# Kernel optimization log

Hardware: AMD Instinct MI355X
Metric: run time of the kernel (lower is better)

The kernel has to match this reference:

```python
import jax, jax.numpy as jnp
import numpy as np
import math

N_HEAD = 16
EPS = 1e-5
GELU_C = math.sqrt(2.0 / math.pi)

def _layernorm(v, w):
    # LN with weight only (bias=None), matching the module's quirky constructor
    mu = jnp.mean(v, axis=-1, keepdims=True)
    var = jnp.mean(jnp.square(v - mu), axis=-1, keepdims=True)
    return (v - mu) * jax.lax.rsqrt(var + EPS) * w

def _new_gelu(x):
    return 0.5 * x * (1.0 + jnp.tanh(GELU_C * (x + 0.044715 * x ** 3)))

def setup_inputs() -> dict:
    key = jax.random.key(0)
    k1, k2, k3, k4 = jax.random.split(key, 4)
    B, T, C = 2, 2048, 2048
    x = jax.random.normal(k1, (B, T, C), dtype=jnp.float32)
    w_qkv = jax.random.normal(k2, (C, 3 * C), dtype=jnp.float32) * 0.02
    w1 = jax.random.normal(k3, (C, 4 * C), dtype=jnp.float32) * 0.02
    w2 = jax.random.normal(k4, (4 * C, C), dtype=jnp.float32) * 0.02
    ln_w = jnp.ones((C,), dtype=jnp.float32)
    return {"x": x, "w_qkv": w_qkv, "w1": w1, "w2": w2, "ln_w": ln_w}

def reference(x, w_qkv, w1, w2, ln_w):
    B, T, C = x.shape
    H = N_HEAD
    D = C // H
    # --- attention branch (pre-LN, shared ln weight) ---
    h = _layernorm(x, ln_w)
    qkv = h @ w_qkv  # [B,T,3C]
    q, k, v = jnp.split(qkv, 3, axis=-1)
    q = q.reshape(B, T, H, D)
    k = k.reshape(B, T, H, D)
    v = v.reshape(B, T, H, D)
    scale = 1.0 / math.sqrt(D)
    att = jnp.einsum('bthd,bshd->bhts', q, k) * scale  # [B,H,T,T]
    causal = jnp.tril(jnp.ones((T, T), dtype=bool))
    att = jnp.where(causal, att, -jnp.inf)
    att = jax.nn.softmax(att, axis=-1)
    attn_out = jnp.einsum('bhts,bshd->bthd', att, v).reshape(B, T, C)
    x = x + attn_out  # note: no output projection in this module
    # --- MLP branch (same ln weight reused) ---
    h2 = _layernorm(x, ln_w)
    mlp = _new_gelu(h2 @ w1) @ w2
    return x + mlp
```

## Files before the change

kernel.cpp:

```cpp
#include <hip/hip_runtime.h>
#include <hip/hip_bf16.h>
#include <math.h>

typedef __bf16 BF16;
typedef __attribute__((ext_vector_type(8))) __bf16 bf16x8;
typedef __attribute__((ext_vector_type(4))) float f32x4;

__device__ __forceinline__ void gld_lds16(const void* g, void* l) {
    __builtin_amdgcn_global_load_lds(
        (__attribute__((address_space(1))) void*)(const void*)g,
        (__attribute__((address_space(3))) void*)l, 16, 0, 0);
}

template <int N> __device__ __forceinline__ void vmwait() {
    if constexpr (N == 0) asm volatile("s_waitcnt vmcnt(0)" ::: "memory");
    else if constexpr (N == 2) asm volatile("s_waitcnt vmcnt(2)" ::: "memory");
    else if constexpr (N == 3) asm volatile("s_waitcnt vmcnt(3)" ::: "memory");
    else if constexpr (N == 4) asm volatile("s_waitcnt vmcnt(4)" ::: "memory");
    else if constexpr (N == 6) asm volatile("s_waitcnt vmcnt(6)" ::: "memory");
    else if constexpr (N == 8) asm volatile("s_waitcnt vmcnt(8)" ::: "memory");
}

__device__ __forceinline__ void barrier_() {
    asm volatile("" ::: "memory");
    __builtin_amdgcn_s_barrier();
    asm volatile("" ::: "memory");
}

__global__ __launch_bounds__(256) void lnorm(const float* __restrict__ x,
                                             const float* __restrict__ w,
                                             BF16* __restrict__ out) {
    const int row = blockIdx.x, tid = threadIdx.x;
    const float* xr = x + (size_t)row * 2048;
    float4 a = *(const float4*)(xr + tid * 8);
    float4 b = *(const float4*)(xr + tid * 8 + 4);
    float s1 = a.x + a.y + a.z + a.w + b.x + b.y + b.z + b.w;
    float s2 = a.x*a.x + a.y*a.y + a.z*a.z + a.w*a.w +
               b.x*b.x + b.y*b.y + b.z*b.z + b.w*b.w;
    #pragma unroll
    for (int off = 32; off; off >>= 1) {
        s1 += __shfl_xor(s1, off);
        s2 += __shfl_xor(s2, off);
    }
    __shared__ float red[8];
    const int l = tid & 63, wv = tid >> 6;
    if (l == 0) { red[wv] = s1; red[4 + wv] = s2; }
    __syncthreads();
    s1 = red[0] + red[1] + red[2] + red[3];
    s2 = red[4] + red[5] + red[6] + red[7];
    const float mean = s1 * (1.0f / 2048.0f);
    const float var  = s2 * (1.0f / 2048.0f) - mean * mean;
    const float rstd = rsqrtf(var + 1e-5f);
    float4 wa = *(const float4*)(w + tid * 8);
    float4 wb = *(const float4*)(w + tid * 8 + 4);
    bf16x8 o;
    o[0] = (BF16)((a.x - mean) * rstd * wa.x);
    o[1] = (BF16)((a.y - mean) * rstd * wa.y);
    o[2] = (BF16)((a.z - mean) * rstd * wa.z);
    o[3] = (BF16)((a.w - mean) * rstd * wa.w);
    o[4] = (BF16)((b.x - mean) * rstd * wb.x);
    o[5] = (BF16)((b.y - mean) * rstd * wb.y);
    o[6] = (BF16)((b.z - mean) * rstd * wb.z);
    o[7] = (BF16)((b.w - mean) * rstd * wb.w);
    *(bf16x8*)(out + (size_t)row * 2048 + tid * 8) = o;
}

__global__ __launch_bounds__(256) void wtrans(const float* __restrict__ W,
                                              BF16* __restrict__ Wt,
                                              int K, int N) {
    __shared__ BF16 tile[32][33];
    const int n0 = blockIdx.x * 32, k0 = blockIdx.y * 32;
    const int tx = threadIdx.x, ty = threadIdx.y;
    #pragma unroll
    for (int i = 0; i < 4; i++)
        tile[ty + 8 * i][tx] = (BF16)W[(size_t)(k0 + ty + 8 * i) * N + n0 + tx];
    __syncthreads();
    #pragma unroll
    for (int i = 0; i < 4; i++)
        Wt[(size_t)(n0 + ty + 8 * i) * K + k0 + tx] = tile[tx][ty + 8 * i];
}

__global__ __launch_bounds__(256) void vtrans(const BF16* __restrict__ qkv,
                                              BF16* __restrict__ vT) {
    __shared__ BF16 tile[32][33];
    const int t0 = blockIdx.x * 32, d0 = blockIdx.y * 32, bh = blockIdx.z;
    const int b = bh >> 4, h = bh & 15;
    const int tx = threadIdx.x, ty = threadIdx.y;
    const BF16* src = qkv + (size_t)b * 2048 * 6144 + 4096 + h * 128;
    #pragma unroll
    for (int i = 0; i < 4; i++)
        tile[ty + 8 * i][tx] = src[(size_t)(t0 + ty + 8 * i) * 6144 + d0 + tx];
    __syncthreads();
    BF16* dst = vT + (size_t)bh * 128 * 2048;
    #pragma unroll
    for (int i = 0; i < 4; i++)
        dst[(size_t)(d0 + ty + 8 * i) * 2048 + t0 + tx] = tile[tx][ty + 8 * i];
}

#define STAGE_A(SB, TS) do { \
    gld_lds16(gA + (size_t)(TS) * 32, lA + (SB) * ABUF); \
    if (LA == 2) gld_lds16(gA + (size_t)(TS) * 32 + (size_t)128 * K, \
                           lA + (SB) * ABUF + 4096); \
} while (0)

#define STAGE_B(SB, TS) do { \
    gld_lds16(gB + (size_t)(TS) * 32, lB + (SB) * BBUF); \
    if (LB == 2) gld_lds16(gB + (size_t)(TS) * 32 + (size_t)128 * K, \
                           lB + (SB) * BBUF + 4096); \
} while (0)

#define TILE(BUF, TS, DS, VM) do { \
    bf16x8 af[MR], bf[NPN]; \
    _Pragma("unroll") \
    for (int m = 0; m < MR; ++m) \
        af[m] = *(const bf16x8*)&As[(BUF) * ABUF + aoff + m * 512]; \
    _Pragma("unroll") \
    for (int n = 0; n < NPN; ++n) \
        bf[n] = *(const bf16x8*)&Bs[(BUF) * BBUF + boff + n * 512]; \
    if (DS) STAGE_A(((BUF) + 3) & 3, TS); \
    if (NPH == 1) { if (DS) STAGE_B(((BUF) + 3) & 3, TS); vmwait<(VM)>(); } \
    barrier_(); \
    __builtin_amdgcn_s_setprio(1); \
    _Pragma("unroll") \
    for (int m = 0; m < MR; ++m) \
      _Pragma("unroll") \
      for (int n = 0; n < NPN; ++n) \
        acc[m][n] = __builtin_amdgcn_mfma_f32_16x16x32_bf16(af[m], bf[n], acc[m][n], 0, 0, 0); \
    __builtin_amdgcn_s_setprio(0); \
    barrier_(); \
    if (NPH == 2) { \
      bf16x8 bf2[NPN]; \
      _Pragma("unroll") \
      for (int n = 0; n < NPN; ++n) \
          bf2[n] = *(const bf16x8*)&Bs[(BUF) * BBUF + boff + (NPN + n) * 512]; \
      if (DS) STAGE_B(((BUF) + 3) & 3, TS); \
      vmwait<(VM)>(); \
      barrier_(); \
      __builtin_amdgcn_s_setprio(1); \
      _Pragma("unroll") \
      for (int m = 0; m < MR; ++m) \
        _Pragma("unroll") \
        for (int n = 0; n < NPN; ++n) \
          acc[m][NPN + n] = __builtin_amdgcn_mfma_f32_16x16x32_bf16(af[m], bf2[n], acc[m][NPN + n], 0, 0, 0); \
      __builtin_amdgcn_s_setprio(0); \
      barrier_(); \
    } \
} while (0)

template <int MODE, int BM, int BN, int WM, int WN>
__global__ __launch_bounds__(512) void gemm8(const BF16* __restrict__ A,
                                             const BF16* __restrict__ Bt,
                                             void* __restrict__ out,
                                             const float* __restrict__ resid,
                                             int M, int N, int K) {
    constexpr int MR  = BM / WM / 16;
    constexpr int NR  = BN / WN / 16;
    constexpr int NPH = (MR * NR) / 16;
    constexpr int NPN = NR / NPH;
    constexpr int LA  = BM / 128;
    constexpr int LB  = BN / 128;
    constexpr int L   = LA + LB;
    constexpr int ABUF = BM * 32;
    constexpr int BBUF = BN * 32;
    (void)M;

    extern __shared__ char smem[];
    BF16* const As = (BF16*)smem;
    BF16* const Bs = As + 4 * ABUF;

    const int tid = threadIdx.x, l = tid & 63, w = tid >> 6;
    const int wm = w / WN, wn = w % WN;
    const int g = l >> 4, c = l & 15;
    const int fa = (c >> 1) & 3;

    const int NBX = N / BN;
    const int cpx = (int)gridDim.x >> 3;
    const int bid = (int)blockIdx.x;
    const int wg  = (bid & 7) * cpx + (bid >> 3);
    const int m0 = (wg / NBX) * BM, n0 = (wg % NBX) * BN;

    const int r0 = tid >> 2;
    const int klog = (tid & 3) ^ ((r0 >> 1) & 3);
    const BF16* const gA = A  + (size_t)(m0 + r0) * K + klog * 8;
    const BF16* const gB = Bt + (size_t)(n0 + r0) * K + klog * 8;
    BF16* const lA = As + w * 512;
    BF16* const lB = Bs + w * 512;

    const int aoff = (wm * (BM / WM) + c) * 32 + ((g ^ fa) << 3);
    const int boff = (wn * (BN / WN) + c) * 32 + ((g ^ fa) << 3);

    f32x4 acc[MR][NR] = {};

    STAGE_A(0, 0); STAGE_B(0, 0);
    STAGE_A(1, 1); STAGE_B(1, 1);
    STAGE_A(2, 2); STAGE_B(2, 2);
    vmwait<2 * L>();
    barrier_();

    const int NT = K >> 5;
    for (int t = 0; t < NT - 4; t += 4) {
        TILE(0, t + 3, true, 2 * L);
        TILE(1, t + 4, true, 2 * L);
        TILE(2, t + 5, true, 2 * L);
        TILE(3, t + 6, true, 2 * L);
    }
    TILE(0, NT - 1, true, 2 * L);
    TILE(1, 0, false, L);
    TILE(2, 0, false, 0);
    TILE(3, 0, false, -1);

    #pragma unroll
    for (int mi = 0; mi < MR; mi++)
      #pragma unroll
      for (int ni = 0; ni < NR; ni++)
        #pragma unroll
        for (int j = 0; j < 4; j++) {
            const int row = m0 + wm * (BM / WM) + mi * 16 + g * 4 + j;
            const int col = n0 + wn * (BN / WN) + ni * 16 + c;
            const float v = acc[mi][ni][j];
            const size_t idx = (size_t)row * N + col;
            if (MODE == 0) {
                ((BF16*)out)[idx] = (BF16)v;
            } else if (MODE == 1) {
                const float t2 = v + 0.044715f * v * v * v;
                const float s = 1.0f / (1.0f + __expf(-1.5957691216057308f * t2));
                ((BF16*)out)[idx] = (BF16)(v * s);
            } else {
                ((float*)out)[idx] = resid[idx] + v;
            }
        }
}

__global__ __launch_bounds__(256) void attn(const BF16* __restrict__ qkv,
                                            const BF16* __restrict__ vT,
                                            const float* __restrict__ x,
                                            float* __restrict__ x2) {
    __shared__ BF16 Ks[2][64 * 128];
    __shared__ BF16 Vs[2][128 * 64];
    __shared__ BF16 Ps[4][16 * 72];
    const int tid = threadIdx.x, l = tid & 63, w = tid >> 6;
    const int g = l >> 4, c = l & 15;
    const int bid = (int)blockIdx.x;
    const int wg = (bid & 7) * 64 + (bid >> 3);
    const int pair = wg & 15, bh = wg >> 4;
    const int b = bh >> 4, h = bh & 15;
    const int xr = (c & 7) << 4;

    const BF16* qbase = qkv + (size_t)b * 2048 * 6144 + h * 128;
    const char* kbase = (const char*)(qbase + 2048);
    const char* vbase = (const char*)(vT + (size_t)bh * 128 * 2048);

    auto STAGE = [&](int bb, int k0) {
        #pragma unroll
        for (int s = 0; s < 4; ++s) {
            const int rK = (w * 4 + s) * 4 + (l >> 4);
            const int cK = ((l & 15) * 16) ^ ((rK & 7) << 4);
            gld_lds16(kbase + (size_t)(k0 + rK) * 12288 + cK,
                      &Ks[bb][(w * 4 + s) * 512]);
            const int rV = (w * 4 + s) * 8 + (l >> 3);
            const int cV = ((l & 7) * 16) ^ ((rV & 7) << 4);
            gld_lds16(vbase + (size_t)rV * 4096 + (size_t)k0 * 2 + cV,
                      &Vs[bb][(w * 4 + s) * 512]);
        }
    };

    const float scale = 0.08838834764831845f;

    #pragma unroll 1
    for (int seg = 0; seg < 2; ++seg) {
        const int qb = seg ? 31 - pair : pair;
        const int q0 = qb * 64;

        bf16x8 qf[4];
        {
            const BF16* qrow = qbase + (size_t)(q0 + w * 16 + c) * 6144 + g * 8;
            #pragma unroll
            for (int kc = 0; kc < 4; kc++)
                qf[kc] = *(const bf16x8*)(qrow + kc * 32);
        }
        float m[4]    = {-1e30f, -1e30f, -1e30f, -1e30f};
        float lsum[4] = {0.f, 0.f, 0.f, 0.f};
        f32x4 O[8] = {};

        STAGE(0, 0);
        #pragma unroll 1
        for (int kt = 0; kt <= qb; ++kt) {
            if (kt < qb) { STAGE((kt + 1) & 1, (kt + 1) * 64); vmwait<8>(); }
            else vmwait<0>();
            barrier_();
            const char* KsB = (const char*)Ks[kt & 1];
            const char* VsB = (const char*)Vs[kt & 1];

            f32x4 s4[4] = {};
            #pragma unroll
            for (int ni = 0; ni < 4; ni++)
                #pragma unroll
                for (int kc = 0; kc < 4; kc++) {
                    const bf16x8 kf = *(const bf16x8*)(KsB +
                        (ni * 16 + c) * 256 + ((kc * 64 + g * 16) ^ xr));
                    s4[ni] = __builtin_amdgcn_mfma_f32_16x16x32_bf16(
                        qf[kc], kf, s4[ni], 0, 0, 0);
                }

            const bool maskt = (kt == qb);
            float sv[4][4];
            #pragma unroll
            for (int ni = 0; ni < 4; ni++)
                #pragma unroll
                for (int j = 0; j < 4; j++) {
                    const float v = s4[ni][j] * scale;
                    sv[ni][j] = (!maskt || (ni * 16 + c <= w * 16 + g * 4 + j))
                              ? v : -1e30f;
                }

            float sf[4];
            #pragma unroll
            for (int j = 0; j < 4; j++) {
                float tm = fmaxf(fmaxf(sv[0][j], sv[1][j]),
                                 fmaxf(sv[2][j], sv[3][j]));
                tm = fmaxf(tm, __shfl_xor(tm, 1));
                tm = fmaxf(tm, __shfl_xor(tm, 2));
                tm = fmaxf(tm, __shfl_xor(tm, 4));
                tm = fmaxf(tm, __shfl_xor(tm, 8));
                const float mn = fmaxf(m[j], tm);
                sf[j] = __expf(m[j] - mn);
                m[j] = mn;
            }

            float rs[4] = {0.f, 0.f, 0.f, 0.f};
            #pragma unroll
            for (int ni = 0; ni < 4; ni++)
                #pragma unroll
                for (int j = 0; j < 4; j++) {
                    const float p = __expf(sv[ni][j] - m[j]);
                    rs[j] += p;
                    Ps[w][(g * 4 + j) * 72 + ni * 16 + c] = (BF16)p;
                }
            #pragma unroll
            for (int j = 0; j < 4; j++) {
                float t = rs[j];
                t += __shfl_xor(t, 1);
                t += __shfl_xor(t, 2);
                t += __shfl_xor(t, 4);
                t += __shfl_xor(t, 8);
                lsum[j] = lsum[j] * sf[j] + t;
            }
            #pragma unroll
            for (int dn = 0; dn < 8; dn++)
                #pragma unroll
                for (int j = 0; j < 4; j++) O[dn][j] *= sf[j];

            bf16x8 pa[2];
            #pragma unroll
            for (int ks = 0; ks < 2; ks++)
                pa[ks] = *(const bf16x8*)((const char*)Ps[w] +
                             c * 144 + ks * 64 + g * 16);
            #pragma unroll
            for (int dn = 0; dn < 8; dn++)
                #pragma unroll
                for (int ks = 0; ks < 2; ks++) {
                    const bf16x8 vf = *(const bf16x8*)(VsB +
                        (dn * 16 + c) * 128 + ((ks * 64 + g * 16) ^ xr));
                    O[dn] = __builtin_amdgcn_mfma_f32_16x16x32_bf16(
                        pa[ks], vf, O[dn], 0, 0, 0);
                }
            barrier_();
        }

        float inv[4];
        #pragma unroll
        for (int j = 0; j < 4; j++) inv[j] = 1.0f / lsum[j];
        #pragma unroll
        for (int dn = 0; dn < 8; dn++)
            #pragma unroll
            for (int j = 0; j < 4; j++) {
                const int t   = q0 + w * 16 + g * 4 + j;
                const int col = h * 128 + dn * 16 + c;
                const size_t idx = ((size_t)b * 2048 + t) * 2048 + col;
                x2[idx] = x[idx] + O[dn][j] * inv[j];
            }
    }
}

extern "C" void kernel_launch(void* const* d_in, const int* in_sizes, int n_in,
                              void* d_out, int out_size, void* d_ws, size_t ws_size,
                              hipStream_t stream) {
    const float* x     = (const float*)d_in[0];
    const float* w_qkv = (const float*)d_in[1];
    const float* w1    = (const float*)d_in[2];
    const float* w2    = (const float*)d_in[3];
    const float* ln_w  = (const float*)d_in[4];
    float* out = (float*)d_out;

    char* ws = (char*)d_ws;
    BF16* h_buf = (BF16*)ws;  ws += (size_t)4096 * 2048 * 2;
    BF16* qkvb  = (BF16*)ws;  ws += (size_t)4096 * 6144 * 2;
    BF16* vTb   = (BF16*)ws;  ws += (size_t)32 * 128 * 2048 * 2;
    BF16* wqkvT = (BF16*)ws;  ws += (size_t)6144 * 2048 * 2;
    BF16* w1T   = (BF16*)ws;  ws += (size_t)8192 * 2048 * 2;
    BF16* w2T   = (BF16*)ws;  ws += (size_t)2048 * 8192 * 2;
    BF16* mlp1  = (BF16*)ws;  ws += (size_t)4096 * 8192 * 2;

    hipFuncSetAttribute((const void*)&gemm8<0, 256, 256, 2, 4>,
                        hipFuncAttributeMaxDynamicSharedMemorySize, 131072);
    hipFuncSetAttribute((const void*)&gemm8<1, 256, 256, 2, 4>,
                        hipFuncAttributeMaxDynamicSharedMemorySize, 131072);
    hipFuncSetAttribute((const void*)&gemm8<2, 256, 128, 4, 2>,
                        hipFuncAttributeMaxDynamicSharedMemorySize, 98304);

    lnorm<<<4096, 256, 0, stream>>>(x, ln_w, h_buf);
    wtrans<<<dim3(192, 64), dim3(32, 8), 0, stream>>>(w_qkv, wqkvT, 2048, 6144);
    gemm8<0, 256, 256, 2, 4><<<384, 512, 131072, stream>>>(
        h_buf, wqkvT, qkvb, nullptr, 4096, 6144, 2048);
    vtrans<<<dim3(64, 4, 32), dim3(32, 8), 0, stream>>>(qkvb, vTb);
    attn<<<512, 256, 0, stream>>>(qkvb, vTb, x, out);

    lnorm<<<4096, 256, 0, stream>>>(out, ln_w, h_buf);
    wtrans<<<dim3(256, 64), dim3(32, 8), 0, stream>>>(w1, w1T, 2048, 8192);
    gemm8<1, 256, 256, 2, 4><<<512, 512, 131072, stream>>>(
        h_buf, w1T, mlp1, nullptr, 4096, 8192, 2048);
    wtrans<<<dim3(64, 256), dim3(32, 8), 0, stream>>>(w2, w2T, 8192, 2048);
    gemm8<2, 256, 128, 4, 2><<<256, 512, 98304, stream>>>(
        mlp1, w2T, out, out, 4096, 2048, 8192);
}
```

Baseline: 556.0 us.

## Replace GEMM with double-buffered BK=64 kernel interleaving loads across quarter-phases

The GEMM kernel is rewritten to use 64-wide K tiles with two LDS buffers instead of 32-wide K tiles with four buffers. Each iteration is split into four MFMA phases, and global-to-LDS loads for the next tile are spread across those phases. The LDS layout gains an XOR swizzle over 128-byte rows for A. The goal is fewer barriers per unit of K and better overlap of memory loads with MFMA work. In exchange, only two stages are in flight, and the hand-tuned vmcnt waits must exactly match the issued load counts.

```diff
diff --git a/kernel.cpp b/kernel.cpp
--- a/kernel.cpp
+++ b/kernel.cpp
@@ -14,10 +14,10 @@
 
 template <int N> __device__ __forceinline__ void vmwait() {
     if constexpr (N == 0) asm volatile("s_waitcnt vmcnt(0)" ::: "memory");
+    else if constexpr (N == 1) asm volatile("s_waitcnt vmcnt(1)" ::: "memory");
     else if constexpr (N == 2) asm volatile("s_waitcnt vmcnt(2)" ::: "memory");
     else if constexpr (N == 3) asm volatile("s_waitcnt vmcnt(3)" ::: "memory");
     else if constexpr (N == 4) asm volatile("s_waitcnt vmcnt(4)" ::: "memory");
-    else if constexpr (N == 6) asm volatile("s_waitcnt vmcnt(6)" ::: "memory");
     else if constexpr (N == 8) asm volatile("s_waitcnt vmcnt(8)" ::: "memory");
 }
 
@@ -97,126 +97,125 @@
         dst[(size_t)(d0 + ty + 8 * i) * 2048 + t0 + tx] = tile[tx][ty + 8 * i];
 }
 
-#define STAGE_A(SB, TS) do { \
-    gld_lds16(gA + (size_t)(TS) * 32, lA + (SB) * ABUF); \
-    if (LA == 2) gld_lds16(gA + (size_t)(TS) * 32 + (size_t)128 * K, \
-                           lA + (SB) * ABUF + 4096); \
+
+#define LDA(BI, M_, MH, KK) ({ \
+    const int r_ = wm * 64 + (M_) * 16 + c; \
+    *(const bf16x8*)(Ab + (BI) * 32768 + (MH) * 16384 + r_ * 128 + \
+                     ((((KK) * 4 + g) ^ (r_ & 7)) << 4)); })
+
+#define LDB(BI, N_, KK) ({ \
+    const int r_ = wn * (BN / 4) + (N_) * 16 + c; \
+    *(const bf16x8*)(Bb + (BI) * BBUF + (KK) * BKU + r_ * 64 + \
+                     ((g ^ (r_ & 3)) << 4)); })
+
+#define STA(SI, MH, TS) do { \
+    _Pragma("unroll") \
+    for (int j_ = 0; j_ < 2; ++j_) { \
+        const int r_ = j_ * 64 + (tid >> 3); \
+        const int sl_ = (tid & 7) ^ (r_ & 7); \
+        gld_lds16(A + (size_t)(m0 + (MH) * 128 + r_) * K + (TS) * 64 + sl_ * 8, \
+                  Ab + (SI) * 32768 + (MH) * 16384 + j_ * 8192 + w * 1024); \
+    } \
 } while (0)
 
-#define STAGE_B(SB, TS) do { \
-    gld_lds16(gB + (size_t)(TS) * 32, lB + (SB) * BBUF); \
-    if (LB == 2) gld_lds16(gB + (size_t)(TS) * 32 + (size_t)128 * K, \
-                           lB + (SB) * BBUF + 4096); \
+#define STB(SI, KU, TS) do { \
+    _Pragma("unroll") \
+    for (int j_ = 0; j_ < LBU; ++j_) { \
+        const int r_ = j_ * 128 + (tid >> 2); \
+        const int sl_ = (tid & 3) ^ (r_ & 3); \
+        gld_lds16(Bt + (size_t)(n0 + r_) * K + (TS) * 64 + (KU) * 32 + sl_ * 8, \
+                  Bb + (SI) * BBUF + (KU) * BKU + j_ * 8192 + w * 1024); \
+    } \
 } while (0)
 
-#define TILE(BUF, TS, DS, VM) do { \
-    bf16x8 af[MR], bf[NPN]; \
-    _Pragma("unroll") \
-    for (int m = 0; m < MR; ++m) \
-        af[m] = *(const bf16x8*)&As[(BUF) * ABUF + aoff + m * 512]; \
-    _Pragma("unroll") \
-    for (int n = 0; n < NPN; ++n) \
-        bf[n] = *(const bf16x8*)&Bs[(BUF) * BBUF + boff + n * 512]; \
-    if (DS) STAGE_A(((BUF) + 3) & 3, TS); \
-    if (NPH == 1) { if (DS) STAGE_B(((BUF) + 3) & 3, TS); vmwait<(VM)>(); } \
-    barrier_(); \
+#define MFMA_CL(MH, AF, BF) do { \
     __builtin_amdgcn_s_setprio(1); \
     _Pragma("unroll") \
-    for (int m = 0; m < MR; ++m) \
+    for (int m_ = 0; m_ < 4; ++m_) \
       _Pragma("unroll") \
-      for (int n = 0; n < NPN; ++n) \
-        acc[m][n] = __builtin_amdgcn_mfma_f32_16x16x32_bf16(af[m], bf[n], acc[m][n], 0, 0, 0); \
+      for (int n_ = 0; n_ < NR; ++n_) \
+        acc[(MH) * 4 + m_][n_] = __builtin_amdgcn_mfma_f32_16x16x32_bf16( \
+            (AF)[m_], (BF)[n_], acc[(MH) * 4 + m_][n_], 0, 0, 0); \
     __builtin_amdgcn_s_setprio(0); \
-    barrier_(); \
-    if (NPH == 2) { \
-      bf16x8 bf2[NPN]; \
-      _Pragma("unroll") \
-      for (int n = 0; n < NPN; ++n) \
-          bf2[n] = *(const bf16x8*)&Bs[(BUF) * BBUF + boff + (NPN + n) * 512]; \
-      if (DS) STAGE_B(((BUF) + 3) & 3, TS); \
-      vmwait<(VM)>(); \
-      barrier_(); \
-      __builtin_amdgcn_s_setprio(1); \
-      _Pragma("unroll") \
-      for (int m = 0; m < MR; ++m) \
-        _Pragma("unroll") \
-        for (int n = 0; n < NPN; ++n) \
-          acc[m][NPN + n] = __builtin_amdgcn_mfma_f32_16x16x32_bf16(af[m], bf2[n], acc[m][NPN + n], 0, 0, 0); \
-      __builtin_amdgcn_s_setprio(0); \
-      barrier_(); \
-    } \
 } while (0)
 
-template <int MODE, int BM, int BN, int WM, int WN>
-__global__ __launch_bounds__(512) void gemm8(const BF16* __restrict__ A,
+#define GBODY(BI, T, ST) do { \
+    bf16x8 bfr[NR], af[4]; \
+    _Pragma("unroll") for (int n_ = 0; n_ < NR; ++n_) bfr[n_] = LDB(BI, n_, 0); \
+    _Pragma("unroll") for (int m_ = 0; m_ < 4; ++m_) af[m_] = LDA(BI, m_, 0, 0); \
+    if (ST) STB((BI) ^ 1, 0, (T) + 1); \
+    barrier_(); \
+    MFMA_CL(0, af, bfr); \
+    if (ST) vmwait<2 * LBU>(); else vmwait<0>(); \
+    barrier_(); \
+    _Pragma("unroll") for (int m_ = 0; m_ < 4; ++m_) af[m_] = LDA(BI, m_, 1, 0); \
+    if (ST) STA((BI) ^ 1, 0, (T) + 1); \
+    barrier_(); \
+    MFMA_CL(1, af, bfr); \
+    if (ST) vmwait<LBU + 2>(); \
+    barrier_(); \
+    _Pragma("unroll") for (int n_ = 0; n_ < NR; ++n_) bfr[n_] = LDB(BI, n_, 1); \
+    _Pragma("unroll") for (int m_ = 0; m_ < 4; ++m_) af[m_] = LDA(BI, m_, 0, 1); \
+    if (ST) STA((BI) ^ 1, 1, (T) + 1); \
+    barrier_(); \
+    MFMA_CL(0, af, bfr); \
+    barrier_(); \
+    _Pragma("unroll") for (int m_ = 0; m_ < 4; ++m_) af[m_] = LDA(BI, m_, 1, 1); \
+    if (ST) STB((BI) ^ 1, 1, (T) + 1); \
+    barrier_(); \
+    MFMA_CL(1, af, bfr); \
+    if (ST) vmwait<LBU + 2>(); \
+    barrier_(); \
+} while (0)
+
+template <int MODE, int BN>
+__global__ __launch_bounds__(512) void gemmT(const BF16* __restrict__ A,
                                              const BF16* __restrict__ Bt,
                                              void* __restrict__ out,
                                              const float* __restrict__ resid,
                                              int M, int N, int K) {
-    constexpr int MR  = BM / WM / 16;
-    constexpr int NR  = BN / WN / 16;
-    constexpr int NPH = (MR * NR) / 16;
-    constexpr int NPN = NR / NPH;
-    constexpr int LA  = BM / 128;
-    constexpr int LB  = BN / 128;
-    constexpr int L   = LA + LB;
-    constexpr int ABUF = BM * 32;
-    constexpr int BBUF = BN * 32;
+    constexpr int NR   = BN / 64;
+    constexpr int LBU  = BN / 128;
+    constexpr int BKU  = BN * 64;
+    constexpr int BBUF = BN * 128;
     (void)M;
 
     extern __shared__ char smem[];
-    BF16* const As = (BF16*)smem;
-    BF16* const Bs = As + 4 * ABUF;
+    char* const Ab = smem;
+    char* const Bb = smem + 65536;
 
     const int tid = threadIdx.x, l = tid & 63, w = tid >> 6;
-    const int wm = w / WN, wn = w % WN;
+    const int wm = w >> 2, wn = w & 3;
     const int g = l >> 4, c = l & 15;
-    const int fa = (c >> 1) & 3;
 
     const int NBX = N / BN;
     const int cpx = (int)gridDim.x >> 3;
     const int bid = (int)blockIdx.x;
     const int wg  = (bid & 7) * cpx + (bid >> 3);
-    const int m0 = (wg / NBX) * BM, n0 = (wg % NBX) * BN;
-
-    const int r0 = tid >> 2;
-    const int klog = (tid & 3) ^ ((r0 >> 1) & 3);
-    const BF16* const gA = A  + (size_t)(m0 + r0) * K + klog * 8;
-    const BF16* const gB = Bt + (size_t)(n0 + r0) * K + klog * 8;
-    BF16* const lA = As + w * 512;
-    BF16* const lB = Bs + w * 512;
-
-    const int aoff = (wm * (BM / WM) + c) * 32 + ((g ^ fa) << 3);
-    const int boff = (wn * (BN / WN) + c) * 32 + ((g ^ fa) << 3);
-
-    f32x4 acc[MR][NR] = {};
-
-    STAGE_A(0, 0); STAGE_B(0, 0);
-    STAGE_A(1, 1); STAGE_B(1, 1);
-    STAGE_A(2, 2); STAGE_B(2, 2);
-    vmwait<2 * L>();
+    const int m0 = (wg / NBX) * 256, n0 = (wg % NBX) * BN;
+
+    f32x4 acc[8][NR] = {};
+
+    STB(0, 0, 0); STA(0, 0, 0); STA(0, 1, 0); STB(0, 1, 0);
+    vmwait<LBU + 2>();
     barrier_();
 
-    const int NT = K >> 5;
-    for (int t = 0; t < NT - 4; t += 4) {
-        TILE(0, t + 3, true, 2 * L);
-        TILE(1, t + 4, true, 2 * L);
-        TILE(2, t + 5, true, 2 * L);
-        TILE(3, t + 6, true, 2 * L);
+    const int NT = K >> 6;
+    for (int t = 0; t < NT - 2; t += 2) {
+        GBODY(0, t, true);
+        GBODY(1, t + 1, true);
     }
-    TILE(0, NT - 1, true, 2 * L);
-    TILE(1, 0, false, L);
-    TILE(2, 0, false, 0);
-    TILE(3, 0, false, -1);
-
-    #pragma unroll
-    for (int mi = 0; mi < MR; mi++)
+    GBODY(0, NT - 2, true);
+    GBODY(1, NT - 1, false);
+
+    #pragma unroll
+    for (int mi = 0; mi < 8; mi++)
       #pragma unroll
       for (int ni = 0; ni < NR; ni++)
         #pragma unroll
         for (int j = 0; j < 4; j++) {
-            const int row = m0 + wm * (BM / WM) + mi * 16 + g * 4 + j;
-            const int col = n0 + wn * (BN / WN) + ni * 16 + c;
+            const int row = m0 + (mi >> 2) * 128 + wm * 64 + (mi & 3) * 16 + g * 4 + j;
+            const int col = n0 + wn * (BN / 4) + ni * 16 + c;
             const float v = acc[mi][ni][j];
             const size_t idx = (size_t)row * N + col;
             if (MODE == 0) {
@@ -401,25 +400,25 @@
     BF16* w2T   = (BF16*)ws;  ws += (size_t)2048 * 8192 * 2;
     BF16* mlp1  = (BF16*)ws;  ws += (size_t)4096 * 8192 * 2;
 
-    hipFuncSetAttribute((const void*)&gemm8<0, 256, 256, 2, 4>,
+    hipFuncSetAttribute((const void*)&gemmT<0, 256>,
                         hipFuncAttributeMaxDynamicSharedMemorySize, 131072);
-    hipFuncSetAttribute((const void*)&gemm8<1, 256, 256, 2, 4>,
+    hipFuncSetAttribute((const void*)&gemmT<1, 256>,
                         hipFuncAttributeMaxDynamicSharedMemorySize, 131072);
-    hipFuncSetAttribute((const void*)&gemm8<2, 256, 128, 4, 2>,
+    hipFuncSetAttribute((const void*)&gemmT<2, 128>,
                         hipFuncAttributeMaxDynamicSharedMemorySize, 98304);
 
     lnorm<<<4096, 256, 0, stream>>>(x, ln_w, h_buf);
     wtrans<<<dim3(192, 64), dim3(32, 8), 0, stream>>>(w_qkv, wqkvT, 2048, 6144);
-    gemm8<0, 256, 256, 2, 4><<<384, 512, 131072, stream>>>(
+    gemmT<0, 256><<<384, 512, 131072, stream>>>(
         h_buf, wqkvT, qkvb, nullptr, 4096, 6144, 2048);
     vtrans<<<dim3(64, 4, 32), dim3(32, 8), 0, stream>>>(qkvb, vTb);
     attn<<<512, 256, 0, stream>>>(qkvb, vTb, x, out);
 
     lnorm<<<4096, 256, 0, stream>>>(out, ln_w, h_buf);
     wtrans<<<dim3(256, 64), dim3(32, 8), 0, stream>>>(w1, w1T, 2048, 8192);
-    gemm8<1, 256, 256, 2, 4><<<512, 512, 131072, stream>>>(
+    gemmT<1, 256><<<512, 512, 131072, stream>>>(
         h_buf, w1T, mlp1, nullptr, 4096, 8192, 2048);
     wtrans<<<dim3(64, 256), dim3(32, 8), 0, stream>>>(w2, w2T, 8192, 2048);
-    gemm8<2, 256, 128, 4, 2><<<256, 512, 98304, stream>>>(
+    gemmT<2, 128><<<256, 512, 98304, stream>>>(
         mlp1, w2T, out, out, 4096, 2048, 8192);
 }
```

New measurement: 557.5 us. About the same (+0.3%).
